# Performance work log

Hardware: AMD Instinct MI355X
Metric: run time of the kernel (lower is better)

Reference implementation:

```python
import jax, jax.numpy as jnp
import numpy as np

V, E, H, S, B = 32000, 1024, 1024, 1024, 64


def setup_inputs() -> dict:
    key = jax.random.key(0)
    ks = jax.random.split(key, 10)
    inp = {
        "word_input": jax.random.randint(ks[0], (1, B), 0, V),
        "last_context": jax.random.normal(ks[1], (B, H), jnp.float32),
        "last_hidden": jax.random.normal(ks[2], (1, B, H), jnp.float32),
        "encoder_outputs": jax.random.normal(ks[3], (S, B, H), jnp.float32),
        # parameters
        "emb_table": jax.random.normal(ks[4], (V, E), jnp.float32) * 0.02,
        "w_ih": jax.random.normal(ks[5], (3 * H, E + H), jnp.float32) * (1.0 / np.sqrt(E + H)),
        "w_hh": jax.random.normal(ks[6], (3 * H, H), jnp.float32) * (1.0 / np.sqrt(H)),
        "b_ih": jnp.zeros((3 * H,), jnp.float32),
        "b_hh": jnp.zeros((3 * H,), jnp.float32),
        "out_W": jax.random.uniform(ks[7], (V, 2 * H), jnp.float32, -0.1, 0.1),
        "out_b": jnp.zeros((V,), jnp.float32),
    }
    return inp


def _gru_step(x, h, w_ih, w_hh, b_ih, b_hh):
    # PyTorch GRU gate order: r, z, n
    gi = x @ w_ih.T + b_ih  # (B, 3H)
    gh = h @ w_hh.T + b_hh  # (B, 3H)
    gi_r, gi_z, gi_n = jnp.split(gi, 3, axis=1)
    gh_r, gh_z, gh_n = jnp.split(gh, 3, axis=1)
    r = jax.nn.sigmoid(gi_r + gh_r)
    z = jax.nn.sigmoid(gi_z + gh_z)
    n = jnp.tanh(gi_n + r * gh_n)
    return (1.0 - z) * n + z * h


def reference(word_input, last_context, last_hidden, encoder_outputs,
              emb_table, w_ih, w_hh, b_ih, b_hh, out_W, out_b):
    # embedding: (1, B, E)
    word_embedded = emb_table[word_input]
    # rnn input: (B, E+H)
    x0 = jnp.concatenate([word_embedded[0], last_context], axis=1)
    h = _gru_step(x0, last_hidden[0], w_ih, w_hh, b_ih, b_hh)  # (B, H)
    hidden = h[None]  # (1, B, H)
    # Luong dot attention, fused: energies (S, B)
    energies = jnp.einsum('bh,sbh->sb', h, encoder_outputs)
    weights = jax.nn.softmax(energies, axis=0)  # softmax over seq dim
    attn_weights = weights.T[:, None, :]  # (B, 1, S)
    context = jnp.einsum('sb,sbh->bh', weights, encoder_outputs)  # (B, H)
    logits = jnp.concatenate([h, context], axis=1) @ out_W.T + out_b  # (B, V)
    output = jax.nn.log_softmax(logits, axis=1)
    return output, context, hidden, attn_weights
```

## Files before the change

kernel.cpp:

```cpp
#include <hip/hip_runtime.h>
#include <math.h>

#define NV 32000
#define NE 1024
#define NH 1024
#define NS 1024
#define NB 64

typedef __attribute__((ext_vector_type(4))) float f32x4;
typedef __attribute__((ext_vector_type(8))) short bf16x8;

#define OUT_CTX   (NB*NV)
#define OUT_HID   (NB*NV + NB*NH)
#define OUT_ATTN  (NB*NV + 2*NB*NH)

#define WS_XA   0
#define WS_HA   (WS_XA + 65536)
#define WS_PG   (WS_HA + 32768)
#define WS_E    (WS_PG + 12*3072*64)
#define WS_PCTX (WS_E + NB*NS)
#define WS_ML   (WS_PCTX + 64*64*1024)
#define WS_LA   (WS_ML + 8192)
#define WS_ML2  (WS_LA + 65536)
#define WS_LSE  (WS_ML2 + 64*2048*2)

__device__ inline unsigned short f2bf(float f) {
    unsigned u = __builtin_bit_cast(unsigned, f);
    u += 0x7fffu + ((u >> 16) & 1u);
    return (unsigned short)(u >> 16);
}

__device__ inline bf16x8 cvt8(float4 a, float4 b) {
    bf16x8 r;
    r[0] = (short)f2bf(a.x); r[1] = (short)f2bf(a.y);
    r[2] = (short)f2bf(a.z); r[3] = (short)f2bf(a.w);
    r[4] = (short)f2bf(b.x); r[5] = (short)f2bf(b.y);
    r[6] = (short)f2bf(b.z); r[7] = (short)f2bf(b.w);
    return r;
}

__device__ inline void store_bf4(unsigned short* p, float4 v) {
    ushort4 u = make_ushort4(f2bf(v.x), f2bf(v.y), f2bf(v.z), f2bf(v.w));
    *(ushort4*)p = u;
}

__global__ void k_prep(const int* __restrict__ wi, const float* __restrict__ lctx,
                       const float* __restrict__ lhid, const float* __restrict__ emb,
                       float* __restrict__ ws) {
    int b = blockIdx.x, t = threadIdx.x;
    unsigned short* XA = (unsigned short*)(ws + WS_XA);
    unsigned short* HA = (unsigned short*)(ws + WS_HA);
    long row = wi[b];
    float4 e4 = ((const float4*)(emb + row*NE))[t];
    float4 c4 = ((const float4*)(lctx + (long)b*NH))[t];
    float4 h4 = ((const float4*)(lhid + (long)b*NH))[t];
    store_bf4(XA + (long)b*2048 + t*4,        e4);
    store_bf4(XA + (long)b*2048 + 1024 + t*4, c4);
    store_bf4(HA + (long)b*1024 + t*4,        h4);
}

__global__ void __launch_bounds__(256) k_gru_mfma(const float* __restrict__ w_ih,
                                                  const float* __restrict__ w_hh,
                                                  float* __restrict__ ws) {
    int wave = blockIdx.x*4 + (threadIdx.x >> 6);
    int lane = threadIdx.x & 63;
    int c = wave % 12, ntile = wave / 12;
    int n0 = ntile * 16;
    int col = lane & 15, kg = lane >> 4;
    const unsigned short* XA = (const unsigned short*)(ws + WS_XA);
    const unsigned short* HA = (const unsigned short*)(ws + WS_HA);
    const float* Wp; const unsigned short* Ap; int ld, kbase;
    if (c < 8) { Wp = w_ih; Ap = XA; ld = 2048; kbase = c*256; }
    else       { Wp = w_hh; Ap = HA; ld = 1024; kbase = (c-8)*256; }
    const float* wrow = Wp + (long)(n0 + col)*ld + kbase + kg*8;
    f32x4 acc[4];
    #pragma unroll
    for (int m = 0; m < 4; m++) acc[m] = (f32x4){0.f,0.f,0.f,0.f};
    #pragma unroll 4
    for (int k0 = 0; k0 < 256; k0 += 32) {
        float4 wa = *(const float4*)(wrow + k0);
        float4 wb = *(const float4*)(wrow + k0 + 4);
        bf16x8 bf = cvt8(wa, wb);
        #pragma unroll
        for (int m = 0; m < 4; m++) {
            bf16x8 af = *(const bf16x8*)(Ap + (long)(m*16 + col)*ld + kbase + k0 + kg*8);
            acc[m] = __builtin_amdgcn_mfma_f32_16x16x32_bf16(af, bf, acc[m], 0, 0, 0);
        }
    }
    float* pg = ws + WS_PG + ((long)c*3072 + n0 + col)*64;
    #pragma unroll
    for (int m = 0; m < 4; m++)
        #pragma unroll
        for (int j = 0; j < 4; j++)
            pg[m*16 + kg*4 + j] = acc[m][j];
}

__global__ void k_gates(const float* __restrict__ wsc, const float* __restrict__ b_ih,
                        const float* __restrict__ b_hh, const float* __restrict__ lhid,
                        float* __restrict__ out, float* __restrict__ ws) {
    int g = blockIdx.x*256 + threadIdx.x;
    int b = g & 63, i = g >> 6;
    float gir=0.f, giz=0.f, gin=0.f, ghr=0.f, ghz=0.f, ghn=0.f;
    #pragma unroll
    for (int c = 0; c < 8; c++) {
        long base = WS_PG + (long)c*3072*64;
        gir += wsc[base + ((long)(0*NH + i))*64 + b];
        giz += wsc[base + ((long)(1*NH + i))*64 + b];
        gin += wsc[base + ((long)(2*NH + i))*64 + b];
    }
    #pragma unroll
    for (int c = 8; c < 12; c++) {
        long base = WS_PG + (long)c*3072*64;
        ghr += wsc[base + ((long)(0*NH + i))*64 + b];
        ghz += wsc[base + ((long)(1*NH + i))*64 + b];
        ghn += wsc[base + ((long)(2*NH + i))*64 + b];
    }
    gir += b_ih[i];        ghr += b_hh[i];
    giz += b_ih[NH + i];   ghz += b_hh[NH + i];
    gin += b_ih[2*NH + i]; ghn += b_hh[2*NH + i];
    float r = 1.f / (1.f + expf(-(gir + ghr)));
    float z = 1.f / (1.f + expf(-(giz + ghz)));
    float n = tanhf(gin + r*ghn);
    float hp = lhid[(long)b*NH + i];
    float h = (1.f - z)*n + z*hp;
    out[OUT_HID + (long)b*NH + i] = h;
    ((unsigned short*)(ws + WS_LA))[(long)b*2048 + i] = f2bf(h);
}

__global__ void __launch_bounds__(256) k_attn(const float* __restrict__ enc,
                                              const float* __restrict__ out,
                                              float* __restrict__ ws) {
    int widx = threadIdx.x >> 6, lane = threadIdx.x & 63;
    int b = blockIdx.x >> 4;
    int g = (blockIdx.x & 15)*4 + widx;
    const float4* hr = (const float4*)(out + OUT_HID + (long)b*NH);
    float4 h0 = hr[lane], h1 = hr[64+lane], h2 = hr[128+lane], h3 = hr[192+lane];
    float m = -1e30f, l = 0.f;
    float4 c0 = make_float4(0,0,0,0), c1 = c0, c2 = c0, c3 = c0;
    const float4* vp = (const float4*)(enc + ((long)(g*16)*NB + b)*NH);
    const long sstr = (long)NB*NH/4;
    float4 a0 = vp[lane], a1 = vp[64+lane], a2 = vp[128+lane], a3 = vp[192+lane];
    #pragma unroll
    for (int si = 0; si < 16; si++) {
        float4 n0 = a0, n1 = a1, n2 = a2, n3 = a3;
        if (si < 15) {
            const float4* np = vp + (long)(si+1)*sstr;
            n0 = np[lane]; n1 = np[64+lane]; n2 = np[128+lane]; n3 = np[192+lane];
        }
        float d = a0.x*h0.x + a0.y*h0.y + a0.z*h0.z + a0.w*h0.w
                + a1.x*h1.x + a1.y*h1.y + a1.z*h1.z + a1.w*h1.w
                + a2.x*h2.x + a2.y*h2.y + a2.z*h2.z + a2.w*h2.w
                + a3.x*h3.x + a3.y*h3.y + a3.z*h3.z + a3.w*h3.w;
        #pragma unroll
        for (int o = 32; o > 0; o >>= 1) d += __shfl_xor(d, o);
        if (lane == 0) ws[WS_E + (long)b*NS + g*16 + si] = d;
        float mnew = fmaxf(m, d);
        float coef = expf(m - mnew);
        float p = expf(d - mnew);
        l = l*coef + p;
        c0.x = c0.x*coef + p*a0.x; c0.y = c0.y*coef + p*a0.y;
        c0.z = c0.z*coef + p*a0.z; c0.w = c0.w*coef + p*a0.w;
        c1.x = c1.x*coef + p*a1.x; c1.y = c1.y*coef + p*a1.y;
        c1.z = c1.z*coef + p*a1.z; c1.w = c1.w*coef + p*a1.w;
        c2.x = c2.x*coef + p*a2.x; c2.y = c2.y*coef + p*a2.y;
        c2.z = c2.z*coef + p*a2.z; c2.w = c2.w*coef + p*a2.w;
        c3.x = c3.x*coef + p*a3.x; c3.y = c3.y*coef + p*a3.y;
        c3.z = c3.z*coef + p*a3.z; c3.w = c3.w*coef + p*a3.w;
        m = mnew;
        a0 = n0; a1 = n1; a2 = n2; a3 = n3;
    }
    float* pc = ws + WS_PCTX + ((long)b*64 + g)*1024;
    *(float4*)(pc + 0*256 + lane*4) = c0;
    *(float4*)(pc + 1*256 + lane*4) = c1;
    *(float4*)(pc + 2*256 + lane*4) = c2;
    *(float4*)(pc + 3*256 + lane*4) = c3;
    if (lane == 0) {
        ws[WS_ML + ((long)b*64 + g)*2]     = m;
        ws[WS_ML + ((long)b*64 + g)*2 + 1] = l;
    }
}

__global__ void k_attn_reduce(const float* __restrict__ wsc, float* __restrict__ out,
                              float* __restrict__ ws) {
    int b = blockIdx.x >> 2, q = blockIdx.x & 3;
    int t = threadIdx.x;
    __shared__ float sm[64], sl[64], sc[64];
    __shared__ float sM, sinvL;
    if (t < 64) {
        sm[t] = wsc[WS_ML + ((long)b*64 + t)*2];
        sl[t] = wsc[WS_ML + ((long)b*64 + t)*2 + 1];
    }
    __syncthreads();
    if (t == 0) {
        float M = -1e30f;
        for (int g = 0; g < 64; g++) M = fmaxf(M, sm[g]);
        float L = 0.f;
        for (int g = 0; g < 64; g++) L += sl[g]*expf(sm[g] - M);
        sM = M; sinvL = 1.f/L;
    }
    __syncthreads();
    float M = sM, invL = sinvL;
    if (t < 64) sc[t] = expf(sm[t] - M);
    __syncthreads();
    int h = q*256 + t;
    float acc = 0.f;
    #pragma unroll 8
    for (int g = 0; g < 64; g++)
        acc += sc[g] * wsc[WS_PCTX + ((long)b*64 + g)*1024 + h];
    float ctx = acc * invL;
    out[OUT_CTX + (long)b*NH + h] = ctx;
    ((unsigned short*)(ws + WS_LA))[(long)b*2048 + 1024 + h] = f2bf(ctx);
    int s = q*256 + t;
    float e = wsc[WS_E + (long)b*NS + s];
    out[OUT_ATTN + (long)b*NS + s] = expf(e - M)*invL;
}

__global__ void __launch_bounds__(64) k_logits_mfma(const float* __restrict__ oW,
                                                    const float* __restrict__ ob,
                                                    const float* __restrict__ wsc,
                                                    float* __restrict__ out,
                                                    float* __restrict__ ws) {
    int vt = blockIdx.x;
    int lane = threadIdx.x & 63;
    int v0 = vt * 16;
    int col = lane & 15, kg = lane >> 4;
    const unsigned short* LA = (const unsigned short*)(wsc + WS_LA);
    const float* wrow = oW + (long)(v0 + col)*2048 + kg*8;
    f32x4 acc[4];
    #pragma unroll
    for (int m = 0; m < 4; m++) acc[m] = (f32x4){0.f,0.f,0.f,0.f};
    #pragma unroll 4
    for (int k0 = 0; k0 < 2048; k0 += 32) {
        float4 wa = *(const float4*)(wrow + k0);
        float4 wb = *(const float4*)(wrow + k0 + 4);
        bf16x8 bf = cvt8(wa, wb);
        #pragma unroll
        for (int m = 0; m < 4; m++) {
            bf16x8 af = *(const bf16x8*)(LA + (long)(m*16 + col)*2048 + k0 + kg*8);
            acc[m] = __builtin_amdgcn_mfma_f32_16x16x32_bf16(af, bf, acc[m], 0, 0, 0);
        }
    }
    float bias = ob[v0 + col];
    #pragma unroll
    for (int m = 0; m < 4; m++) {
        #pragma unroll
        for (int j = 0; j < 4; j++) {
            int row = m*16 + kg*4 + j;
            float v = acc[m][j] + bias;
            out[(long)row*NV + v0 + col] = v;
            float mx = v;
            mx = fmaxf(mx, __shfl_xor(mx, 1));
            mx = fmaxf(mx, __shfl_xor(mx, 2));
            mx = fmaxf(mx, __shfl_xor(mx, 4));
            mx = fmaxf(mx, __shfl_xor(mx, 8));
            float p = expf(v - mx);
            p += __shfl_xor(p, 1);
            p += __shfl_xor(p, 2);
            p += __shfl_xor(p, 4);
            p += __shfl_xor(p, 8);
            if (col == 0)
                *(float2*)(ws + WS_ML2 + ((long)row*2048 + vt)*2) = make_float2(mx, p);
        }
    }
}

__global__ void __launch_bounds__(1024) k_lse(const float* __restrict__ wsc,
                                              float* __restrict__ ws) {
    int b = blockIdx.x, t = threadIdx.x;
    __shared__ float sm_[1024], sl_[1024];
    const float2* ml = (const float2*)(wsc + WS_ML2 + (long)b*4096);
    float m = -1e30f, l = 0.f;
    for (int c = t; c < 2000; c += 1024) {
        float2 v = ml[c];
        float mn = fmaxf(m, v.x);
        l = l*expf(m - mn) + v.y*expf(v.x - mn);
        m = mn;
    }
    sm_[t] = m; sl_[t] = l; __syncthreads();
    for (int o = 512; o > 0; o >>= 1) {
        if (t < o) {
            float m2 = sm_[t+o], l2 = sl_[t+o];
            float mn = fmaxf(sm_[t], m2);
            sl_[t] = sl_[t]*expf(sm_[t] - mn) + l2*expf(m2 - mn);
            sm_[t] = mn;
        }
        __syncthreads();
    }
    if (t == 0) ws[WS_LSE + b] = sm_[0] + logf(sl_[0]);
}

__global__ void __launch_bounds__(1024) k_norm(const float* __restrict__ wsc,
                                               float* __restrict__ out) {
    int g = blockIdx.x*1024 + threadIdx.x;
    int b = g / 8000;
    int i = g - b*8000;
    float lse = wsc[WS_LSE + b];
    float4* p = (float4*)(out + (long)b*NV) + i;
    float4 v = *p;
    *p = make_float4(v.x-lse, v.y-lse, v.z-lse, v.w-lse);
}

extern "C" void kernel_launch(void* const* d_in, const int* in_sizes, int n_in,
                              void* d_out, int out_size, void* d_ws, size_t ws_size,
                              hipStream_t stream) {
    const int*   wi   = (const int*)d_in[0];
    const float* lctx = (const float*)d_in[1];
    const float* lhid = (const float*)d_in[2];
    const float* enc  = (const float*)d_in[3];
    const float* emb  = (const float*)d_in[4];
    const float* w_ih = (const float*)d_in[5];
    const float* w_hh = (const float*)d_in[6];
    const float* b_ih = (const float*)d_in[7];
    const float* b_hh = (const float*)d_in[8];
    const float* oW   = (const float*)d_in[9];
    const float* ob   = (const float*)d_in[10];
    float* out = (float*)d_out;
    float* ws  = (float*)d_ws;

    hipLaunchKernelGGL(k_prep,        dim3(64),   dim3(256),  0, stream, wi, lctx, lhid, emb, ws);
    hipLaunchKernelGGL(k_gru_mfma,    dim3(576),  dim3(256),  0, stream, w_ih, w_hh, ws);
    hipLaunchKernelGGL(k_gates,       dim3(256),  dim3(256),  0, stream, ws, b_ih, b_hh, lhid, out, ws);
    hipLaunchKernelGGL(k_attn,        dim3(1024), dim3(256),  0, stream, enc, out, ws);
    hipLaunchKernelGGL(k_attn_reduce, dim3(256),  dim3(256),  0, stream, ws, out, ws);
    hipLaunchKernelGGL(k_logits_mfma, dim3(2000), dim3(64),   0, stream, oW, ob, ws, out, ws);
    hipLaunchKernelGGL(k_lse,         dim3(64),   dim3(1024), 0, stream, ws, ws);
    hipLaunchKernelGGL(k_norm,        dim3(500),  dim3(1024), 0, stream, ws, out);
}
```

Before: 219.0 us.

## Split logits GEMM by K and overlap hidden half with attention kernel

The output projection is split along K: the half that depends only on the GRU hidden state is computed inside the attention kernel by extra blocks, which write partial logits to workspace. The later logits kernel then handles only the context half and adds the stored partials. This is meant to overlap the bandwidth-heavy out_W reads with the encoder streaming and halve the critical-path work after attention. The online softmax also gets a lazy-rescale rule (rescale only when the max grows by more than 8), which cuts exp and multiply work. The cost is an extra partial-logits buffer to write and read back, and looser bounds on the running accumulators.

```diff
diff --git a/kernel.cpp b/kernel.cpp
--- a/kernel.cpp
+++ b/kernel.cpp
@@ -23,6 +23,7 @@
 #define WS_LA   (WS_ML + 8192)
 #define WS_ML2  (WS_LA + 65536)
 #define WS_LSE  (WS_ML2 + 64*2048*2)
+#define WS_P    (WS_LSE + 64)
 
 __device__ inline unsigned short f2bf(float f) {
     unsigned u = __builtin_bit_cast(unsigned, f);
@@ -127,12 +128,42 @@
     ((unsigned short*)(ws + WS_LA))[(long)b*2048 + i] = f2bf(h);
 }
 
-__global__ void __launch_bounds__(256) k_attn(const float* __restrict__ enc,
-                                              const float* __restrict__ out,
-                                              float* __restrict__ ws) {
+__global__ void __launch_bounds__(256) k_attn_logh(const float* __restrict__ enc,
+                                                   const float* __restrict__ oW,
+                                                   const float* __restrict__ out,
+                                                   float* __restrict__ ws) {
     int widx = threadIdx.x >> 6, lane = threadIdx.x & 63;
-    int b = blockIdx.x >> 4;
-    int g = (blockIdx.x & 15)*4 + widx;
+    if (blockIdx.x < 500) {
+        int vt = blockIdx.x*4 + widx;
+        int v0 = vt * 16;
+        int col = lane & 15, kg = lane >> 4;
+        const unsigned short* LA = (const unsigned short*)(ws + WS_LA);
+        const float* wrow = oW + (long)(v0 + col)*2048 + kg*8;
+        f32x4 acc[4];
+        #pragma unroll
+        for (int m = 0; m < 4; m++) acc[m] = (f32x4){0.f,0.f,0.f,0.f};
+        #pragma unroll 4
+        for (int k0 = 0; k0 < 1024; k0 += 32) {
+            float4 wa = *(const float4*)(wrow + k0);
+            float4 wb = *(const float4*)(wrow + k0 + 4);
+            bf16x8 bf = cvt8(wa, wb);
+            #pragma unroll
+            for (int m = 0; m < 4; m++) {
+                bf16x8 af = *(const bf16x8*)(LA + (long)(m*16 + col)*2048 + k0 + kg*8);
+                acc[m] = __builtin_amdgcn_mfma_f32_16x16x32_bf16(af, bf, acc[m], 0, 0, 0);
+            }
+        }
+        float* P = ws + WS_P + (long)vt*1024;
+        #pragma unroll
+        for (int m = 0; m < 4; m++)
+            #pragma unroll
+            for (int j = 0; j < 4; j++)
+                P[(m*16 + kg*4 + j)*16 + col] = acc[m][j];
+        return;
+    }
+    int blk = blockIdx.x - 500;
+    int b = blk >> 4;
+    int g = (blk & 15)*4 + widx;
     const float4* hr = (const float4*)(out + OUT_HID + (long)b*NH);
     float4 h0 = hr[lane], h1 = hr[64+lane], h2 = hr[128+lane], h3 = hr[192+lane];
     float m = -1e30f, l = 0.f;
@@ -154,19 +185,21 @@
         #pragma unroll
         for (int o = 32; o > 0; o >>= 1) d += __shfl_xor(d, o);
         if (lane == 0) ws[WS_E + (long)b*NS + g*16 + si] = d;
-        float mnew = fmaxf(m, d);
-        float coef = expf(m - mnew);
-        float p = expf(d - mnew);
-        l = l*coef + p;
-        c0.x = c0.x*coef + p*a0.x; c0.y = c0.y*coef + p*a0.y;
-        c0.z = c0.z*coef + p*a0.z; c0.w = c0.w*coef + p*a0.w;
-        c1.x = c1.x*coef + p*a1.x; c1.y = c1.y*coef + p*a1.y;
-        c1.z = c1.z*coef + p*a1.z; c1.w = c1.w*coef + p*a1.w;
-        c2.x = c2.x*coef + p*a2.x; c2.y = c2.y*coef + p*a2.y;
-        c2.z = c2.z*coef + p*a2.z; c2.w = c2.w*coef + p*a2.w;
-        c3.x = c3.x*coef + p*a3.x; c3.y = c3.y*coef + p*a3.y;
-        c3.z = c3.z*coef + p*a3.z; c3.w = c3.w*coef + p*a3.w;
-        m = mnew;
+        if (d > m + 8.f) {
+            float coef = expf(m - d);
+            l *= coef;
+            c0.x *= coef; c0.y *= coef; c0.z *= coef; c0.w *= coef;
+            c1.x *= coef; c1.y *= coef; c1.z *= coef; c1.w *= coef;
+            c2.x *= coef; c2.y *= coef; c2.z *= coef; c2.w *= coef;
+            c3.x *= coef; c3.y *= coef; c3.z *= coef; c3.w *= coef;
+            m = d;
+        }
+        float p = expf(d - m);
+        l += p;
+        c0.x += p*a0.x; c0.y += p*a0.y; c0.z += p*a0.z; c0.w += p*a0.w;
+        c1.x += p*a1.x; c1.y += p*a1.y; c1.z += p*a1.z; c1.w += p*a1.w;
+        c2.x += p*a2.x; c2.y += p*a2.y; c2.z += p*a2.z; c2.w += p*a2.w;
+        c3.x += p*a3.x; c3.y += p*a3.y; c3.z += p*a3.z; c3.w += p*a3.w;
         a0 = n0; a1 = n1; a2 = n2; a3 = n3;
     }
     float* pc = ws + WS_PCTX + ((long)b*64 + g)*1024;
@@ -215,38 +248,39 @@
     out[OUT_ATTN + (long)b*NS + s] = expf(e - M)*invL;
 }
 
-__global__ void __launch_bounds__(64) k_logits_mfma(const float* __restrict__ oW,
+__global__ void __launch_bounds__(256) k_logits_ctx(const float* __restrict__ oW,
                                                     const float* __restrict__ ob,
                                                     const float* __restrict__ wsc,
                                                     float* __restrict__ out,
                                                     float* __restrict__ ws) {
-    int vt = blockIdx.x;
-    int lane = threadIdx.x & 63;
+    int widx = threadIdx.x >> 6, lane = threadIdx.x & 63;
+    int vt = blockIdx.x*4 + widx;
     int v0 = vt * 16;
     int col = lane & 15, kg = lane >> 4;
     const unsigned short* LA = (const unsigned short*)(wsc + WS_LA);
-    const float* wrow = oW + (long)(v0 + col)*2048 + kg*8;
+    const float* wrow = oW + (long)(v0 + col)*2048 + 1024 + kg*8;
     f32x4 acc[4];
     #pragma unroll
     for (int m = 0; m < 4; m++) acc[m] = (f32x4){0.f,0.f,0.f,0.f};
     #pragma unroll 4
-    for (int k0 = 0; k0 < 2048; k0 += 32) {
+    for (int k0 = 0; k0 < 1024; k0 += 32) {
         float4 wa = *(const float4*)(wrow + k0);
         float4 wb = *(const float4*)(wrow + k0 + 4);
         bf16x8 bf = cvt8(wa, wb);
         #pragma unroll
         for (int m = 0; m < 4; m++) {
-            bf16x8 af = *(const bf16x8*)(LA + (long)(m*16 + col)*2048 + k0 + kg*8);
+            bf16x8 af = *(const bf16x8*)(LA + (long)(m*16 + col)*2048 + 1024 + k0 + kg*8);
             acc[m] = __builtin_amdgcn_mfma_f32_16x16x32_bf16(af, bf, acc[m], 0, 0, 0);
         }
     }
+    const float* P = wsc + WS_P + (long)vt*1024;
     float bias = ob[v0 + col];
     #pragma unroll
     for (int m = 0; m < 4; m++) {
         #pragma unroll
         for (int j = 0; j < 4; j++) {
             int row = m*16 + kg*4 + j;
-            float v = acc[m][j] + bias;
+            float v = acc[m][j] + P[row*16 + col] + bias;
             out[(long)row*NV + v0 + col] = v;
             float mx = v;
             mx = fmaxf(mx, __shfl_xor(mx, 1));
@@ -320,9 +354,9 @@
     hipLaunchKernelGGL(k_prep,        dim3(64),   dim3(256),  0, stream, wi, lctx, lhid, emb, ws);
     hipLaunchKernelGGL(k_gru_mfma,    dim3(576),  dim3(256),  0, stream, w_ih, w_hh, ws);
     hipLaunchKernelGGL(k_gates,       dim3(256),  dim3(256),  0, stream, ws, b_ih, b_hh, lhid, out, ws);
-    hipLaunchKernelGGL(k_attn,        dim3(1024), dim3(256),  0, stream, enc, out, ws);
+    hipLaunchKernelGGL(k_attn_logh,   dim3(1524), dim3(256),  0, stream, enc, oW, out, ws);
     hipLaunchKernelGGL(k_attn_reduce, dim3(256),  dim3(256),  0, stream, ws, out, ws);
-    hipLaunchKernelGGL(k_logits_mfma, dim3(2000), dim3(64),   0, stream, oW, ob, ws, out, ws);
+    hipLaunchKernelGGL(k_logits_ctx,  dim3(500),  dim3(256),  0, stream, oW, ob, ws, out, ws);
     hipLaunchKernelGGL(k_lse,         dim3(64),   dim3(1024), 0, stream, ws, ws);
     hipLaunchKernelGGL(k_norm,        dim3(500),  dim3(1024), 0, stream, ws, out);
 }
```

New measurement: 213.1 us. 1.03x faster.
